# Kernel tuning notes

Measured on AMD Instinct MI355X. Metric: run time of the kernel, lower is better.

The kernel has to match this reference:

```python
import jax, jax.numpy as jnp
import numpy as np

N_NODES = 50000
N_EDGES = 400000
D_IN = 128
D_H = 128
N_CLASSES = 20
N_GRAPHS = 256
EPS_BN = 1e-5


def _lin_params(key, d_in, d_out, scale=0.05):
    kw, kb = jax.random.split(key)
    W = jax.random.normal(kw, (d_in, d_out), jnp.float32) * scale
    b = jax.random.normal(kb, (d_out,), jnp.float32) * scale
    return W, b


def setup_inputs() -> dict:
    key = jax.random.key(0)
    ks = jax.random.split(key, 20)
    inp = {
        "x": jax.random.normal(ks[0], (N_NODES, D_IN), jnp.float32),
        "edge_index": jax.random.randint(ks[1], (2, N_EDGES), 0, N_NODES, jnp.int32),
        "batch": jnp.sort(jax.random.randint(ks[2], (N_NODES,), 0, N_GRAPHS, jnp.int32)),
    }
    kidx = 3
    for li, d_in in zip((1, 2, 3), (D_IN, D_H, D_H)):
        for nm in ("q", "k", "v", "s"):
            W, b = _lin_params(ks[kidx], d_in, D_H)
            kidx += 1
            inp[f"W{nm}{li}"] = W
            inp[f"b{nm}{li}"] = b
        inp[f"gamma{li}"] = jnp.ones((D_H,), jnp.float32)
        inp[f"beta{li}"] = jnp.zeros((D_H,), jnp.float32)
    Wl, bl = _lin_params(ks[kidx], D_H, N_CLASSES)
    inp["Wlin"] = Wl
    inp["blin"] = bl
    return inp


def _segment_softmax(logits, seg, n):
    m = jax.ops.segment_max(logits, seg, num_segments=n)
    e = jnp.exp(logits - m[seg])
    s = jax.ops.segment_sum(e, seg, num_segments=n)
    return e / (s[seg] + 1e-16)


def _transformer_conv(x, src, dst, Wq, bq, Wk, bk, Wv, bv, Ws, bs):
    # heads=1, concat=True, root_weight=True (PyG TransformerConv defaults)
    q = x @ Wq + bq  # [N, d]
    k = x @ Wk + bk
    v = x @ Wv + bv
    d = q.shape[-1]
    logits = jnp.sum(q[dst] * k[src], axis=-1) / jnp.sqrt(jnp.float32(d))  # [E]
    alpha = _segment_softmax(logits, dst, x.shape[0])
    out = jax.ops.segment_sum(alpha[:, None] * v[src], dst, num_segments=x.shape[0])
    return out + x @ Ws + bs


def _batch_norm(x, gamma, beta):
    mu = jnp.mean(x, axis=0)
    var = jnp.var(x, axis=0)
    return gamma * (x - mu) * jax.lax.rsqrt(var + EPS_BN) + beta


def _global_mean_pool(x, batch, n_graphs):
    sums = jax.ops.segment_sum(x, batch, num_segments=n_graphs)
    cnt = jax.ops.segment_sum(jnp.ones((x.shape[0],), x.dtype), batch, num_segments=n_graphs)
    return sums / jnp.maximum(cnt, 1.0)[:, None]


def reference(x, edge_index, batch,
              Wq1, bq1, Wk1, bk1, Wv1, bv1, Ws1, bs1, gamma1, beta1,
              Wq2, bq2, Wk2, bk2, Wv2, bv2, Ws2, bs2, gamma2, beta2,
              Wq3, bq3, Wk3, bk3, Wv3, bv3, Ws3, bs3, gamma3, beta3,
              Wlin, blin):
    src, dst = edge_index[0], edge_index[1]
    h = _transformer_conv(x, src, dst, Wq1, bq1, Wk1, bk1, Wv1, bv1, Ws1, bs1)
    h = jax.nn.relu(_batch_norm(h, gamma1, beta1))  # dropout inactive (eval)
    h = _transformer_conv(h, src, dst, Wq2, bq2, Wk2, bk2, Wv2, bv2, Ws2, bs2)
    h = jax.nn.relu(_batch_norm(h, gamma2, beta2))
    h = _transformer_conv(h, src, dst, Wq3, bq3, Wk3, bk3, Wv3, bv3, Ws3, bs3)
    h = jax.nn.relu(_batch_norm(h, gamma3, beta3))
    g = _global_mean_pool(h, batch, N_GRAPHS)  # [G, d]
    return g @ Wlin + blin  # [G, num_classes]
```

## Files before the change

### kernel.cpp

```cpp
#include <hip/hip_runtime.h>

#define N_NODES 50000
#define N_EDGES 400000
#define DH 128
#define N_GRAPHS 256

#define SCAN_CHUNK 512
#define N_CHUNKS ((N_NODES + SCAN_CHUNK - 1) / SCAN_CHUNK)
#define ATTN_BLOCKS ((N_NODES + 15) / 16)
#define POOL_CHUNKS ((N_NODES + 63) / 64)
#define PSLOTS 16

typedef __bf16 bf16x8 __attribute__((ext_vector_type(8)));
typedef float f32x4 __attribute__((ext_vector_type(4)));
typedef _Float16 f16x2 __attribute__((ext_vector_type(2)));
typedef _Float16 f16x8 __attribute__((ext_vector_type(8)));

#define DEV __device__ __forceinline__

#if defined(__has_builtin)
#if __has_builtin(__builtin_amdgcn_fdot2)
#define HAS_FDOT2 1
#endif
#endif

DEV float fdot2acc(f16x2 a, f16x2 b, float c) {
#ifdef HAS_FDOT2
  return __builtin_amdgcn_fdot2(a, b, c, false);
#else
  return (float)a.x * (float)b.x + (float)a.y * (float)b.y + c;
#endif
}

DEV unsigned short f2bf(float f) {
  union { float f; unsigned int i; } v; v.f = f;
  unsigned int x = v.i;
  unsigned int r = (x + 0x7fffu + ((x >> 16) & 1u)) >> 16;
  return (unsigned short)r;
}

struct WPtrs { const float* w[12]; };

__global__ void repack_kernel(WPtrs wp, unsigned short* __restrict__ WB) {
  int mat = blockIdx.y;
  int m = blockIdx.x * 256 + threadIdx.x;
  int j = m & 7;
  int lane = (m >> 3) & 63;
  int ct = (m >> 9) & 7;
  int kk = m >> 12;
  int i = kk * 32 + (lane >> 4) * 8 + j;
  int o = ct * 16 + (lane & 15);
  WB[mat * 16384 + m] = f2bf(wp.w[mat][i * 128 + o]);
}

__global__ void deg_count(const int* __restrict__ ei, int* __restrict__ deg, int E) {
  int e = blockIdx.x * 256 + threadIdx.x;
  if (e < E) atomicAdd(&deg[ei[E + e]], 1);
}

__global__ __launch_bounds__(256) void scan_sum(const int* __restrict__ deg,
                                                int* __restrict__ partials, int N) {
  __shared__ int red[256];
  int b = blockIdx.x, t = threadIdx.x;
  int base = b * SCAN_CHUNK + t * 2;
  int s = 0;
  if (base + 1 < N) { int2 v = *reinterpret_cast<const int2*>(deg + base); s = v.x + v.y; }
  else if (base < N) s = deg[base];
  red[t] = s;
  __syncthreads();
  for (int off = 128; off; off >>= 1) {
    if (t < off) red[t] += red[t + off];
    __syncthreads();
  }
  if (t == 0) partials[b] = red[0];
}

__global__ __launch_bounds__(256) void scan_apply(const int* __restrict__ deg,
                                                  const int* __restrict__ partials,
                                                  int* __restrict__ rowptr,
                                                  int* __restrict__ cursor, int N, int E) {
  __shared__ int s[256];
  __shared__ int prefSh;
  int b = blockIdx.x, t = threadIdx.x;

  s[t] = (t < b) ? partials[t] : 0;
  __syncthreads();
  for (int off = 128; off; off >>= 1) {
    if (t < off) s[t] += s[t + off];
    __syncthreads();
  }
  if (t == 0) prefSh = s[0];
  __syncthreads();
  int pref = prefSh;
  __syncthreads();

  int base = b * SCAN_CHUNK + t * 2;
  int d0 = 0, d1 = 0;
  if (base + 1 < N) { int2 v = *reinterpret_cast<const int2*>(deg + base); d0 = v.x; d1 = v.y; }
  else if (base < N) d0 = deg[base];
  int local = d0 + d1;
  s[t] = local;
  __syncthreads();
  for (int off = 1; off < 256; off <<= 1) {
    int o = (t >= off) ? s[t - off] : 0;
    __syncthreads();
    s[t] += o;
    __syncthreads();
  }
  int offp = pref + s[t] - local;
  if (base < N)     { rowptr[base] = offp;          cursor[base] = offp; }
  if (base + 1 < N) { rowptr[base + 1] = offp + d0; cursor[base + 1] = offp + d0; }
  if (b == 0 && t == 0) rowptr[N] = E;
}

__global__ void csr_scatter(const int* __restrict__ ei, int* __restrict__ cursor,
                            int* __restrict__ adj, int E) {
  int e = blockIdx.x * 256 + threadIdx.x;
  if (e < E) {
    int dst = ei[E + e];
    int pos = atomicAdd(&cursor[dst], 1);
    adj[pos] = ei[e];
  }
}

__global__ __launch_bounds__(256) void adj_sort16(const int* __restrict__ rowptr,
                                                  int* __restrict__ adj, int N) {
  __shared__ int buf[16 * 32];
  int t = threadIdx.x;
  int g = t >> 4, l = t & 15;
  int n = blockIdx.x * 16 + g;
  bool valid = n < N;
  int p0 = 0, d = 0;
  if (valid) { p0 = rowptr[n]; d = rowptr[n + 1] - p0; }
  if (__builtin_expect(d > 32, 0)) {
    if (l == 0) {
      for (int i = p0 + 1; i < p0 + d; ++i) {
        int v = adj[i]; int j = i - 1;
        while (j >= p0 && adj[j] > v) { adj[j + 1] = adj[j]; --j; }
        adj[j + 1] = v;
      }
    }
    d = 0;
  }
  int a0 = (l < d) ? adj[p0 + l] : 0x7fffffff;
  int a1 = (16 + l < d) ? adj[p0 + 16 + l] : 0x7fffffff;
  int r0 = 0, r1 = 0;
#pragma unroll
  for (int i = 0; i < 16; ++i) {
    int v0 = __shfl(a0, i, 16);
    int v1 = __shfl(a1, i, 16);
    r0 += (v0 < a0) || (v0 == a0 && i < l);
    r0 += (v1 < a0);
    r1 += (v0 <= a1);
    r1 += (v1 < a1) || (v1 == a1 && i < l);
  }
  if (l < d)      buf[g * 32 + r0] = a0;
  if (16 + l < d) buf[g * 32 + r1] = a1;
  __syncthreads();
  if (l < d)      adj[p0 + l]      = buf[g * 32 + l];
  if (16 + l < d) adj[p0 + 16 + l] = buf[g * 32 + 16 + l];
}

struct GemmOut { _Float16* Y[4]; const float* bias[4]; int ldY[4]; };

#define LDP 136

__global__ __launch_bounds__(256) void gemm_proj(
    const float* __restrict__ Xf,
    const _Float16* __restrict__ Hin,
    const float* __restrict__ scale, const float* __restrict__ shift,
    const unsigned short* __restrict__ WB4,
    GemmOut go, int useBN, int N)
{
  __shared__ __align__(16) unsigned short xs[64 * LDP];

  const int t = threadIdx.x;
  const int rowBase = blockIdx.x * 64;
  const int igc = (t & 15) * 8;

  if (useBN) {
    float4 sc0 = *reinterpret_cast<const float4*>(scale + igc);
    float4 sc1 = *reinterpret_cast<const float4*>(scale + igc + 4);
    float4 sh0 = *reinterpret_cast<const float4*>(shift + igc);
    float4 sh1 = *reinterpret_cast<const float4*>(shift + igc + 4);
#pragma unroll
    for (int j = 0; j < 4; ++j) {
      int v = t + 256 * j;
      int r = v >> 4;
      int grow = rowBase + r;
      ushort4 o0 = make_ushort4(0, 0, 0, 0), o1 = make_ushort4(0, 0, 0, 0);
      if (grow < N) {
        f16x8 hv = *reinterpret_cast<const f16x8*>(Hin + (size_t)grow * 128 + igc);
        o0.x = f2bf(fmaxf((float)hv[0] * sc0.x + sh0.x, 0.f));
        o0.y = f2bf(fmaxf((float)hv[1] * sc0.y + sh0.y, 0.f));
        o0.z = f2bf(fmaxf((float)hv[2] * sc0.z + sh0.z, 0.f));
        o0.w = f2bf(fmaxf((float)hv[3] * sc0.w + sh0.w, 0.f));
        o1.x = f2bf(fmaxf((float)hv[4] * sc1.x + sh1.x, 0.f));
        o1.y = f2bf(fmaxf((float)hv[5] * sc1.y + sh1.y, 0.f));
        o1.z = f2bf(fmaxf((float)hv[6] * sc1.z + sh1.z, 0.f));
        o1.w = f2bf(fmaxf((float)hv[7] * sc1.w + sh1.w, 0.f));
      }
      *reinterpret_cast<ushort4*>(&xs[r * LDP + igc]) = o0;
      *reinterpret_cast<ushort4*>(&xs[r * LDP + igc + 4]) = o1;
    }
  } else {
#pragma unroll
    for (int j = 0; j < 4; ++j) {
      int v = t + 256 * j;
      int r = v >> 4;
      int grow = rowBase + r;
      ushort4 o0 = make_ushort4(0, 0, 0, 0), o1 = make_ushort4(0, 0, 0, 0);
      if (grow < N) {
        float4 a = *reinterpret_cast<const float4*>(Xf + (size_t)grow * 128 + igc);
        float4 b = *reinterpret_cast<const float4*>(Xf + (size_t)grow * 128 + igc + 4);
        o0.x = f2bf(a.x); o0.y = f2bf(a.y); o0.z = f2bf(a.z); o0.w = f2bf(a.w);
        o1.x = f2bf(b.x); o1.y = f2bf(b.y); o1.z = f2bf(b.z); o1.w = f2bf(b.w);
      }
      *reinterpret_cast<ushort4*>(&xs[r * LDP + igc]) = o0;
      *reinterpret_cast<ushort4*>(&xs[r * LDP + igc + 4]) = o1;
    }
  }
  __syncthreads();

  const int wave = t >> 6;
  const int lane = t & 63;
  const int ln16 = lane & 15;
  const int quad = lane >> 4;
  const int r0 = wave * 16;

  bf16x8 afrag[4];
#pragma unroll
  for (int kk = 0; kk < 4; ++kk)
    afrag[kk] = *reinterpret_cast<const bf16x8*>(&xs[(r0 + ln16) * LDP + kk * 32 + quad * 8]);
  __syncthreads();

  for (int proj = 0; proj < 4; ++proj) {
    const unsigned short* __restrict__ WB = WB4 + proj * 16384;
    const float* __restrict__ bias = go.bias[proj];

    f32x4 acc[8] = {};
#pragma unroll
    for (int kk = 0; kk < 4; ++kk) {
#pragma unroll
      for (int ct = 0; ct < 8; ++ct) {
        bf16x8 b = *reinterpret_cast<const bf16x8*>(WB + ((kk * 8 + ct) * 64 + lane) * 8);
        acc[ct] = __builtin_amdgcn_mfma_f32_16x16x32_bf16(afrag[kk], b, acc[ct], 0, 0, 0);
      }
    }

    _Float16* __restrict__ Yh = go.Y[proj];
    const int ldY = go.ldY[proj];
#pragma unroll
    for (int ct = 0; ct < 8; ++ct) {
      int col = ct * 16 + ln16;
      float bv = bias[col];
#pragma unroll
      for (int reg = 0; reg < 4; ++reg) {
        _Float16 hv = (_Float16)(acc[ct][reg] + bv);
        xs[(r0 + quad * 4 + reg) * LDP + col] = __builtin_bit_cast(unsigned short, hv);
      }
    }
#pragma unroll
    for (int pass = 0; pass < 4; ++pass) {
      int rl = (lane >> 4) + pass * 4;
      int grow = rowBase + r0 + rl;
      f16x8 v = *reinterpret_cast<const f16x8*>(&xs[(r0 + rl) * LDP + ln16 * 8]);
      if (grow < N)
        *reinterpret_cast<f16x8*>(&Yh[(size_t)grow * ldY + ln16 * 8]) = v;
    }
  }
}

__global__ __launch_bounds__(256) void node_attn(
    const int* __restrict__ rowptr, const int* __restrict__ adj,
    const _Float16* __restrict__ Q, const _Float16* __restrict__ KV,
    _Float16* __restrict__ H, float* __restrict__ Pbuf, int N)
{
  __shared__ float lsum[16][132];
  __shared__ float lsq[16][132];
  int t = threadIdx.x;
  int w = t >> 4, lane = t & 15;
  int n = blockIdx.x * 16 + w;
  bool valid = n < N;
  int nn = valid ? n : 0;
  int p0 = 0, p1 = 0;
  if (valid) { p0 = rowptr[n]; p1 = rowptr[n + 1]; }
  int d = p1 - p0;

  f16x8 qv = *reinterpret_cast<const f16x8*>(Q + (size_t)nn * 128 + lane * 8);
  f16x8 hh = *reinterpret_cast<const f16x8*>(H + (size_t)nn * 128 + lane * 8);
  f16x2 q0 = {qv[0], qv[1]}, q1 = {qv[2], qv[3]}, q2 = {qv[4], qv[5]}, q3 = {qv[6], qv[7]};

  const float rsqd = 0.08838834764831845f;
  float m = -INFINITY, s = 0.f;
  float acc[8] = {};

#define EDGE1(SRC) do {                                                        \
    const _Float16* bp_ = KV + (size_t)(SRC) * 256 + lane * 8;                 \
    f16x8 ke_ = *reinterpret_cast<const f16x8*>(bp_);                          \
    f16x8 ve_ = *reinterpret_cast<const f16x8*>(bp_ + 128);                    \
    float dd_ = fdot2acc(q0, (f16x2){ke_[0], ke_[1]},                          \
                fdot2acc(q1, (f16x2){ke_[2], ke_[3]},                          \
                fdot2acc(q2, (f16x2){ke_[4], ke_[5]},                          \
                fdot2acc(q3, (f16x2){ke_[6], ke_[7]}, 0.f))));                 \
    for (int off_ = 8; off_; off_ >>= 1) dd_ += __shfl_xor(dd_, off_, 16);     \
    float ll_ = dd_ * rsqd;                                                    \
    float mn_ = fmaxf(m, ll_);                                                 \
    float sc_ = __expf(m - mn_);                                               \
    float w0_ = __expf(ll_ - mn_);                                             \
    for (int i_ = 0; i_ < 8; ++i_) acc[i_] = acc[i_] * sc_ + w0_ * (float)ve_[i_]; \
    s = s * sc_ + w0_;                                                         \
    m = mn_;                                                                   \
  } while (0)

  if (__builtin_expect(d <= 32, 1)) {
    int aLo = (lane < d) ? adj[p0 + lane] : 0;
    int aHi = (16 + lane < d) ? adj[p0 + 16 + lane] : 0;
    int e = 0;
    for (; e + 1 < d; e += 2) {
      int s0 = __shfl((e     < 16) ? aLo : aHi, (e    ) & 15, 16);
      int s1 = __shfl((e + 1 < 16) ? aLo : aHi, (e + 1) & 15, 16);
      const _Float16* b0 = KV + (size_t)s0 * 256 + lane * 8;
      const _Float16* b1 = KV + (size_t)s1 * 256 + lane * 8;
      f16x8 k0 = *reinterpret_cast<const f16x8*>(b0);
      f16x8 k1 = *reinterpret_cast<const f16x8*>(b1);
      f16x8 v0 = *reinterpret_cast<const f16x8*>(b0 + 128);
      f16x8 v1 = *reinterpret_cast<const f16x8*>(b1 + 128);
      float d0 = fdot2acc(q0, (f16x2){k0[0], k0[1]},
                 fdot2acc(q1, (f16x2){k0[2], k0[3]},
                 fdot2acc(q2, (f16x2){k0[4], k0[5]},
                 fdot2acc(q3, (f16x2){k0[6], k0[7]}, 0.f))));
      float d1 = fdot2acc(q0, (f16x2){k1[0], k1[1]},
                 fdot2acc(q1, (f16x2){k1[2], k1[3]},
                 fdot2acc(q2, (f16x2){k1[4], k1[5]},
                 fdot2acc(q3, (f16x2){k1[6], k1[7]}, 0.f))));
#pragma unroll
      for (int off = 8; off; off >>= 1) {
        d0 += __shfl_xor(d0, off, 16);
        d1 += __shfl_xor(d1, off, 16);
      }
      float l0 = d0 * rsqd;
      float l1 = d1 * rsqd;
      float mn = fmaxf(m, fmaxf(l0, l1));
      float sc = __expf(m - mn);
      float w0 = __expf(l0 - mn);
      float w1 = __expf(l1 - mn);
#pragma unroll
      for (int i = 0; i < 8; ++i)
        acc[i] = acc[i] * sc + w0 * (float)v0[i] + w1 * (float)v1[i];
      s = s * sc + w0 + w1;
      m = mn;
    }
    if (e < d) {
      int sE = __shfl((e < 16) ? aLo : aHi, e & 15, 16);
      EDGE1(sE);
    }
  } else {
    for (int p = p0; p < p1; ++p) { int sE = adj[p]; EDGE1(sE); }
  }
#undef EDGE1

  float h[8];
#pragma unroll
  for (int i = 0; i < 8; ++i) h[i] = 0.f;
  if (valid) {
    float inv = 1.0f / (s + 1e-16f);
    f16x8 ho;
#pragma unroll
    for (int i = 0; i < 8; ++i) {
      h[i] = (float)hh[i] + acc[i] * inv;
      ho[i] = (_Float16)h[i];
    }
    *reinterpret_cast<f16x8*>(H + (size_t)n * 128 + lane * 8) = ho;
  }

#pragma unroll
  for (int i = 0; i < 8; i += 4) {
    float4 hv = make_float4(h[i], h[i + 1], h[i + 2], h[i + 3]);
    float4 h2 = make_float4(hv.x * hv.x, hv.y * hv.y, hv.z * hv.z, hv.w * hv.w);
    *reinterpret_cast<float4*>(&lsum[w][lane * 8 + i]) = hv;
    *reinterpret_cast<float4*>(&lsq[w][lane * 8 + i]) = h2;
  }
  __syncthreads();

  int f = t & 127;
  float a = 0.f;
  if (t < 128) {
#pragma unroll
    for (int n16 = 0; n16 < 16; ++n16) a += lsum[n16][f];
  } else {
#pragma unroll
    for (int n16 = 0; n16 < 16; ++n16) a += lsq[n16][f];
  }
  Pbuf[(size_t)blockIdx.x * 256 + t] = a;
}

__global__ __launch_bounds__(256) void bn_fused(
    const float* __restrict__ Pbuf, float* __restrict__ bnpart,
    const float* __restrict__ gamma, const float* __restrict__ beta,
    float* __restrict__ scale, float* __restrict__ shift,
    int* __restrict__ ticket, int N)
{
  __shared__ float red[256];
  __shared__ int amLast;
  int t = threadIdx.x;
  {
    float s0 = 0.f, s1 = 0.f, s2 = 0.f, s3 = 0.f;
    int r = blockIdx.x;
    for (; r + 192 < ATTN_BLOCKS; r += 256) {
      s0 += Pbuf[(size_t)(r      ) * 256 + t];
      s1 += Pbuf[(size_t)(r +  64) * 256 + t];
      s2 += Pbuf[(size_t)(r + 128) * 256 + t];
      s3 += Pbuf[(size_t)(r + 192) * 256 + t];
    }
    for (; r < ATTN_BLOCKS; r += 64) s0 += Pbuf[(size_t)r * 256 + t];
    bnpart[blockIdx.x * 256 + t] = s0 + s1 + s2 + s3;
  }
  __threadfence();
  if (t == 0) amLast = (atomicAdd(ticket, 1) == 63);
  __syncthreads();
  if (!amLast) return;
  __threadfence();

  float s0 = 0.f, s1 = 0.f, s2 = 0.f, s3 = 0.f;
#pragma unroll
  for (int r = 0; r < 64; r += 4) {
    s0 += bnpart[(r + 0) * 256 + t];
    s1 += bnpart[(r + 1) * 256 + t];
    s2 += bnpart[(r + 2) * 256 + t];
    s3 += bnpart[(r + 3) * 256 + t];
  }
  red[t] = s0 + s1 + s2 + s3;
  __syncthreads();
  if (t < 128) {
    float mean = red[t] / (float)N;
    float var = red[t + 128] / (float)N - mean * mean;
    var = fmaxf(var, 0.f);
    float sc = gamma[t] * rsqrtf(var + 1e-5f);
    scale[t] = sc;
    shift[t] = beta[t] - mean * sc;
  }
}

__global__ __launch_bounds__(256) void pool_partial(
    const _Float16* __restrict__ H, const float* __restrict__ scale,
    const float* __restrict__ shift, const int* __restrict__ batch,
    float* __restrict__ partial, int N)
{
  int f = threadIdx.x & 127, parity = threadIdx.x >> 7;
  int base = blockIdx.x * 64;
  int lim = min(base + 64, N);
  float sc = scale[f], sh = shift[f];
  int slot = ((blockIdx.x & 7) << 1) | parity;
  int curg = -1; float s = 0.f;
  for (int row = base + parity; row < lim; row += 2) {
    int g = batch[row];
    if (g != curg) {
      if (curg >= 0) partial[(size_t)((curg << 4) | slot) * 128 + f] = s;
      curg = g; s = 0.f;
    }
    s += fmaxf((float)H[(size_t)row * 128 + f] * sc + sh, 0.f);
  }
  if (curg >= 0) partial[(size_t)((curg << 4) | slot) * 128 + f] = s;
}

__global__ __launch_bounds__(128) void final_linear(
    const float* __restrict__ partial, const int* __restrict__ batch,
    const float* __restrict__ Wlin, const float* __restrict__ blin,
    float* __restrict__ out, int N)
{
  __shared__ float pf[128];
  int g = blockIdx.x;
  int t = threadIdx.x;
  float s = 0.f;
#pragma unroll
  for (int sl = 0; sl < PSLOTS; ++sl)
    s += partial[(size_t)((g << 4) | sl) * 128 + t];
  pf[t] = s;
  __syncthreads();
  int lo = 0, hi = N;
  while (lo < hi) { int mid = (lo + hi) >> 1; if (batch[mid] < g) lo = mid + 1; else hi = mid; }
  int start = lo;
  hi = N;
  while (lo < hi) { int mid = (lo + hi) >> 1; if (batch[mid] < g + 1) lo = mid + 1; else hi = mid; }
  float inv = 1.0f / fmaxf((float)(lo - start), 1.f);
  if (t < 20) {
    float acc = 0.f;
#pragma unroll 4
    for (int i = 0; i < 128; ++i)
      acc += pf[i] * Wlin[i * 20 + t];
    out[g * 20 + t] = acc * inv + blin[t];
  }
}

extern "C" void kernel_launch(void* const* d_in, const int* in_sizes, int n_in,
                              void* d_out, int out_size, void* d_ws, size_t ws_size,
                              hipStream_t stream)
{
  const int N = N_NODES, E = N_EDGES, G = N_GRAPHS;

  const float* x = (const float*)d_in[0];
  const int* ei = (const int*)d_in[1];
  const int* batch = (const int*)d_in[2];
  const float* Wlin = (const float*)d_in[33];
  const float* blin = (const float*)d_in[34];

  char* ws = (char*)d_ws;
  size_t off = 0;
  auto alloc = [&](size_t bytes) -> void* {
    void* p = ws + off;
    off = (off + bytes + 255) & ~(size_t)255;
    return p;
  };
  unsigned short* WB = (unsigned short*)alloc(12 * 16384 * sizeof(unsigned short));
  _Float16* Qh  = (_Float16*)alloc((size_t)N * 128 * 2);
  _Float16* KVh = (_Float16*)alloc((size_t)N * 256 * 2);
  _Float16* Hh  = (_Float16*)alloc((size_t)N * 128 * 2);
  int* rowptr   = (int*)alloc((size_t)(N + 1) * 4);
  int* cursor   = (int*)alloc((size_t)N * 4);
  int* adj      = (int*)alloc((size_t)E * 4);
  int* partials = (int*)alloc((size_t)N_CHUNKS * 4);
  float* Pbuf   = (float*)alloc((size_t)ATTN_BLOCKS * 256 * 4);
  float* bnpart = (float*)alloc((size_t)64 * 256 * 4);
  float* scale  = (float*)alloc(128 * 4);
  float* shift  = (float*)alloc(128 * 4);
  size_t zoff = off;
  int* deg      = (int*)alloc((size_t)N * 4);
  int* tickets  = (int*)alloc(256);
  float* ppool  = (float*)alloc((size_t)G * PSLOTS * 128 * 4);
  size_t zbytes = off - zoff;

  WPtrs wp;
  for (int L = 0; L < 3; ++L) {
    wp.w[L * 4 + 0] = (const float*)d_in[3 + L * 10 + 0];
    wp.w[L * 4 + 1] = (const float*)d_in[3 + L * 10 + 2];
    wp.w[L * 4 + 2] = (const float*)d_in[3 + L * 10 + 4];
    wp.w[L * 4 + 3] = (const float*)d_in[3 + L * 10 + 6];
  }
  repack_kernel<<<dim3(64, 12), 256, 0, stream>>>(wp, WB);

  hipMemsetAsync(deg, 0, zbytes, stream);
  deg_count<<<(E + 255) / 256, 256, 0, stream>>>(ei, deg, E);
  scan_sum<<<N_CHUNKS, 256, 0, stream>>>(deg, partials, N);
  scan_apply<<<N_CHUNKS, 256, 0, stream>>>(deg, partials, rowptr, cursor, N, E);
  csr_scatter<<<(E + 255) / 256, 256, 0, stream>>>(ei, cursor, adj, E);
  adj_sort16<<<ATTN_BLOCKS, 256, 0, stream>>>(rowptr, adj, N);

  for (int L = 0; L < 3; ++L) {
    GemmOut go;
    go.Y[0] = Qh;        go.ldY[0] = 128;
    go.Y[1] = KVh;       go.ldY[1] = 256;
    go.Y[2] = KVh + 128; go.ldY[2] = 256;
    go.Y[3] = Hh;        go.ldY[3] = 128;
    go.bias[0] = (const float*)d_in[3 + L * 10 + 1];
    go.bias[1] = (const float*)d_in[3 + L * 10 + 3];
    go.bias[2] = (const float*)d_in[3 + L * 10 + 5];
    go.bias[3] = (const float*)d_in[3 + L * 10 + 7];
    gemm_proj<<<(N + 63) / 64, 256, 0, stream>>>(
        x, Hh, scale, shift, WB + L * 4 * 16384, go, (L > 0) ? 1 : 0, N);

    node_attn<<<ATTN_BLOCKS, 256, 0, stream>>>(rowptr, adj, Qh, KVh, Hh, Pbuf, N);

    bn_fused<<<64, 256, 0, stream>>>(Pbuf, bnpart,
        (const float*)d_in[3 + L * 10 + 8],
        (const float*)d_in[3 + L * 10 + 9],
        scale, shift, tickets + L, N);

    if (L == 2) {
      pool_partial<<<POOL_CHUNKS, 256, 0, stream>>>(Hh, scale, shift, batch, ppool, N);
      final_linear<<<G, 128, 0, stream>>>(ppool, batch, Wlin, blin, (float*)d_out, N);
    }
  }
}
```

Before: 433.0 us.

## Fold BN reduction, adj sort and zeroing into neighbouring kernels to cut launches

Removes the separate bn_fused kernel by having the last-arriving 64 blocks of the next GEMM (or pool) kernel compute the batch-norm statistics, while every other block spin-waits on a release flag. It also runs the adjacency sort as extra blocks of the first GEMM launch and replaces the memset plus weight-repack kernel with one combined kernel. The aim is to remove several kernel launches and their gaps. The cost is an in-kernel spin barrier. It relies on the late-ranked blocks being resident while the others spin, which risks stalls or deadlock if they are not.

New measurement: 913.2 us. 2.11x slower.

```diff
diff --git a/kernel.cpp b/kernel.cpp
--- a/kernel.cpp
+++ b/kernel.cpp
@@ -9,6 +9,7 @@
 #define N_CHUNKS ((N_NODES + SCAN_CHUNK - 1) / SCAN_CHUNK)
 #define ATTN_BLOCKS ((N_NODES + 15) / 16)
 #define POOL_CHUNKS ((N_NODES + 63) / 64)
+#define NB_GEMM ((N_NODES + 63) / 64)
 #define PSLOTS 16
 
 typedef __bf16 bf16x8 __attribute__((ext_vector_type(8)));
@@ -41,16 +42,27 @@
 
 struct WPtrs { const float* w[12]; };
 
-__global__ void repack_kernel(WPtrs wp, unsigned short* __restrict__ WB) {
-  int mat = blockIdx.y;
-  int m = blockIdx.x * 256 + threadIdx.x;
-  int j = m & 7;
-  int lane = (m >> 3) & 63;
-  int ct = (m >> 9) & 7;
-  int kk = m >> 12;
-  int i = kk * 32 + (lane >> 4) * 8 + j;
-  int o = ct * 16 + (lane & 15);
-  WB[mat * 16384 + m] = f2bf(wp.w[mat][i * 128 + o]);
+__global__ __launch_bounds__(256) void repack_zero(
+    WPtrs wp, unsigned short* __restrict__ WB,
+    int* __restrict__ deg, int* __restrict__ ctrl, float* __restrict__ ppool,
+    int N)
+{
+  const int T = 768 * 256;
+  int gtid = blockIdx.x * 256 + threadIdx.x;
+  for (int m = gtid; m < 12 * 16384; m += T) {
+    int mat = m >> 14;
+    int mm = m & 16383;
+    int j = mm & 7;
+    int lane = (mm >> 3) & 63;
+    int ct = (mm >> 9) & 7;
+    int kk = mm >> 12;
+    int i = kk * 32 + (lane >> 4) * 8 + j;
+    int o = ct * 16 + (lane & 15);
+    WB[m] = f2bf(wp.w[mat][i * 128 + o]);
+  }
+  for (int i = gtid; i < N; i += T) deg[i] = 0;
+  if (gtid < 64) ctrl[gtid] = 0;
+  for (int i = gtid; i < N_GRAPHS * PSLOTS * 128; i += T) ppool[i] = 0.f;
 }
 
 __global__ void deg_count(const int* __restrict__ ei, int* __restrict__ deg, int E) {
@@ -123,12 +135,12 @@
   }
 }
 
-__global__ __launch_bounds__(256) void adj_sort16(const int* __restrict__ rowptr,
-                                                  int* __restrict__ adj, int N) {
-  __shared__ int buf[16 * 32];
+DEV void adj_sort_body(const int* __restrict__ rowptr, int* __restrict__ adj,
+                       int nodeBase, int N) {
+  __shared__ int sbuf[16 * 32];
   int t = threadIdx.x;
   int g = t >> 4, l = t & 15;
-  int n = blockIdx.x * 16 + g;
+  int n = nodeBase + g;
   bool valid = n < N;
   int p0 = 0, d = 0;
   if (valid) { p0 = rowptr[n]; d = rowptr[n + 1] - p0; }
@@ -154,25 +166,95 @@
     r1 += (v0 <= a1);
     r1 += (v1 < a1) || (v1 == a1 && i < l);
   }
-  if (l < d)      buf[g * 32 + r0] = a0;
-  if (16 + l < d) buf[g * 32 + r1] = a1;
-  __syncthreads();
-  if (l < d)      adj[p0 + l]      = buf[g * 32 + l];
-  if (16 + l < d) adj[p0 + 16 + l] = buf[g * 32 + 16 + l];
+  if (l < d)      sbuf[g * 32 + r0] = a0;
+  if (16 + l < d) sbuf[g * 32 + r1] = a1;
+  __syncthreads();
+  if (l < d)      adj[p0 + l]      = sbuf[g * 32 + l];
+  if (16 + l < d) adj[p0 + 16 + l] = sbuf[g * 32 + 16 + l];
+}
+
+DEV void bn_prologue(const float* __restrict__ Pbuf, float* __restrict__ bnpart,
+                     const float* __restrict__ gamma, const float* __restrict__ beta,
+                     float* __restrict__ scale, float* __restrict__ shift,
+                     int* __restrict__ sync, int nb, int N) {
+  __shared__ int rankSh;
+  __shared__ int lastSh;
+  __shared__ float red[256];
+  int t = threadIdx.x;
+  if (t == 0) rankSh = atomicAdd(&sync[0], 1);
+  __syncthreads();
+  int rank = rankSh;
+  if (rank >= nb - 64 && rank < nb) {
+    int slot = rank - (nb - 64);
+    float s0 = 0.f, s1 = 0.f, s2 = 0.f, s3 = 0.f;
+    int r = slot;
+    for (; r + 192 < ATTN_BLOCKS; r += 256) {
+      s0 += Pbuf[(size_t)(r      ) * 256 + t];
+      s1 += Pbuf[(size_t)(r +  64) * 256 + t];
+      s2 += Pbuf[(size_t)(r + 128) * 256 + t];
+      s3 += Pbuf[(size_t)(r + 192) * 256 + t];
+    }
+    for (; r < ATTN_BLOCKS; r += 64) s0 += Pbuf[(size_t)r * 256 + t];
+    bnpart[slot * 256 + t] = s0 + s1 + s2 + s3;
+    __threadfence();
+    if (t == 0) lastSh = (atomicAdd(&sync[1], 1) == 63);
+    __syncthreads();
+    if (lastSh) {
+      __threadfence();
+      float v0 = 0.f, v1 = 0.f, v2 = 0.f, v3 = 0.f;
+#pragma unroll
+      for (int q = 0; q < 64; q += 4) {
+        v0 += bnpart[(q + 0) * 256 + t];
+        v1 += bnpart[(q + 1) * 256 + t];
+        v2 += bnpart[(q + 2) * 256 + t];
+        v3 += bnpart[(q + 3) * 256 + t];
+      }
+      red[t] = v0 + v1 + v2 + v3;
+      __syncthreads();
+      if (t < 128) {
+        float mean = red[t] / (float)N;
+        float var = red[t + 128] / (float)N - mean * mean;
+        var = fmaxf(var, 0.f);
+        float sc = gamma[t] * rsqrtf(var + 1e-5f);
+        scale[t] = sc;
+        shift[t] = beta[t] - mean * sc;
+      }
+      __syncthreads();
+      __threadfence();
+      if (t == 0)
+        __hip_atomic_store(&sync[2], 1, __ATOMIC_RELEASE, __HIP_MEMORY_SCOPE_AGENT);
+    }
+  }
+  if (t == 0) {
+    while (__hip_atomic_load(&sync[2], __ATOMIC_ACQUIRE,
+                             __HIP_MEMORY_SCOPE_AGENT) == 0) {}
+  }
+  __syncthreads();
 }
 
 struct GemmOut { _Float16* Y[4]; const float* bias[4]; int ldY[4]; };
 
 #define LDP 136
 
-__global__ __launch_bounds__(256) void gemm_proj(
+__global__ __launch_bounds__(256, 4) void gemm_proj(
     const float* __restrict__ Xf,
     const _Float16* __restrict__ Hin,
-    const float* __restrict__ scale, const float* __restrict__ shift,
+    const float* __restrict__ Pbuf, float* __restrict__ bnpart,
+    const float* __restrict__ gamma, const float* __restrict__ beta,
+    float* __restrict__ scale, float* __restrict__ shift,
+    int* __restrict__ sync,
     const unsigned short* __restrict__ WB4,
-    GemmOut go, int useBN, int N)
+    GemmOut go, int useBN, int N, int nbGemm,
+    const int* __restrict__ rowptr, int* __restrict__ adj)
 {
   __shared__ __align__(16) unsigned short xs[64 * LDP];
+
+  if ((int)blockIdx.x >= nbGemm) {
+    adj_sort_body(rowptr, adj, ((int)blockIdx.x - nbGemm) * 16, N);
+    return;
+  }
+  if (useBN)
+    bn_prologue(Pbuf, bnpart, gamma, beta, scale, shift, sync, nbGemm, N);
 
   const int t = threadIdx.x;
   const int rowBase = blockIdx.x * 64;
@@ -395,58 +477,16 @@
   Pbuf[(size_t)blockIdx.x * 256 + t] = a;
 }
 
-__global__ __launch_bounds__(256) void bn_fused(
+__global__ __launch_bounds__(256) void pool_partial(
+    const _Float16* __restrict__ H,
     const float* __restrict__ Pbuf, float* __restrict__ bnpart,
     const float* __restrict__ gamma, const float* __restrict__ beta,
     float* __restrict__ scale, float* __restrict__ shift,
-    int* __restrict__ ticket, int N)
+    int* __restrict__ sync,
+    const int* __restrict__ batch, float* __restrict__ partial, int N)
 {
-  __shared__ float red[256];
-  __shared__ int amLast;
-  int t = threadIdx.x;
-  {
-    float s0 = 0.f, s1 = 0.f, s2 = 0.f, s3 = 0.f;
-    int r = blockIdx.x;
-    for (; r + 192 < ATTN_BLOCKS; r += 256) {
-      s0 += Pbuf[(size_t)(r      ) * 256 + t];
-      s1 += Pbuf[(size_t)(r +  64) * 256 + t];
-      s2 += Pbuf[(size_t)(r + 128) * 256 + t];
-      s3 += Pbuf[(size_t)(r + 192) * 256 + t];
-    }
-    for (; r < ATTN_BLOCKS; r += 64) s0 += Pbuf[(size_t)r * 256 + t];
-    bnpart[blockIdx.x * 256 + t] = s0 + s1 + s2 + s3;
-  }
-  __threadfence();
-  if (t == 0) amLast = (atomicAdd(ticket, 1) == 63);
-  __syncthreads();
-  if (!amLast) return;
-  __threadfence();
-
-  float s0 = 0.f, s1 = 0.f, s2 = 0.f, s3 = 0.f;
-#pragma unroll
-  for (int r = 0; r < 64; r += 4) {
-    s0 += bnpart[(r + 0) * 256 + t];
-    s1 += bnpart[(r + 1) * 256 + t];
-    s2 += bnpart[(r + 2) * 256 + t];
-    s3 += bnpart[(r + 3) * 256 + t];
-  }
-  red[t] = s0 + s1 + s2 + s3;
-  __syncthreads();
-  if (t < 128) {
-    float mean = red[t] / (float)N;
-    float var = red[t + 128] / (float)N - mean * mean;
-    var = fmaxf(var, 0.f);
-    float sc = gamma[t] * rsqrtf(var + 1e-5f);
-    scale[t] = sc;
-    shift[t] = beta[t] - mean * sc;
-  }
-}
-
-__global__ __launch_bounds__(256) void pool_partial(
-    const _Float16* __restrict__ H, const float* __restrict__ scale,
-    const float* __restrict__ shift, const int* __restrict__ batch,
-    float* __restrict__ partial, int N)
-{
+  bn_prologue(Pbuf, bnpart, gamma, beta, scale, shift, sync, POOL_CHUNKS, N);
+
   int f = threadIdx.x & 127, parity = threadIdx.x >> 7;
   int base = blockIdx.x * 64;
   int lim = min(base + 64, N);
@@ -524,11 +564,11 @@
   float* bnpart = (float*)alloc((size_t)64 * 256 * 4);
   float* scale  = (float*)alloc(128 * 4);
   float* shift  = (float*)alloc(128 * 4);
-  size_t zoff = off;
   int* deg      = (int*)alloc((size_t)N * 4);
-  int* tickets  = (int*)alloc(256);
+  int* ctrl     = (int*)alloc(64 * 4);
   float* ppool  = (float*)alloc((size_t)G * PSLOTS * 128 * 4);
-  size_t zbytes = off - zoff;
+
+  int* snc[3] = { ctrl + 16, ctrl + 20, ctrl + 24 };
 
   WPtrs wp;
   for (int L = 0; L < 3; ++L) {
@@ -537,14 +577,12 @@
     wp.w[L * 4 + 2] = (const float*)d_in[3 + L * 10 + 4];
     wp.w[L * 4 + 3] = (const float*)d_in[3 + L * 10 + 6];
   }
-  repack_kernel<<<dim3(64, 12), 256, 0, stream>>>(wp, WB);
-
-  hipMemsetAsync(deg, 0, zbytes, stream);
+
+  repack_zero<<<768, 256, 0, stream>>>(wp, WB, deg, ctrl, ppool, N);
   deg_count<<<(E + 255) / 256, 256, 0, stream>>>(ei, deg, E);
   scan_sum<<<N_CHUNKS, 256, 0, stream>>>(deg, partials, N);
   scan_apply<<<N_CHUNKS, 256, 0, stream>>>(deg, partials, rowptr, cursor, N, E);
   csr_scatter<<<(E + 255) / 256, 256, 0, stream>>>(ei, cursor, adj, E);
-  adj_sort16<<<ATTN_BLOCKS, 256, 0, stream>>>(rowptr, adj, N);
 
   for (int L = 0; L < 3; ++L) {
     GemmOut go;
@@ -556,19 +594,27 @@
     go.bias[1] = (const float*)d_in[3 + L * 10 + 3];
     go.bias[2] = (const float*)d_in[3 + L * 10 + 5];
     go.bias[3] = (const float*)d_in[3 + L * 10 + 7];
-    gemm_proj<<<(N + 63) / 64, 256, 0, stream>>>(
-        x, Hh, scale, shift, WB + L * 4 * 16384, go, (L > 0) ? 1 : 0, N);
+
+    if (L == 0) {
+      gemm_proj<<<NB_GEMM + ATTN_BLOCKS, 256, 0, stream>>>(
+          x, Hh, nullptr, nullptr, nullptr, nullptr, scale, shift, snc[0],
+          WB, go, 0, N, NB_GEMM, rowptr, adj);
+    } else {
+      gemm_proj<<<NB_GEMM, 256, 0, stream>>>(
+          x, Hh, Pbuf, bnpart,
+          (const float*)d_in[3 + (L - 1) * 10 + 8],
+          (const float*)d_in[3 + (L - 1) * 10 + 9],
+          scale, shift, snc[L - 1],
+          WB + L * 4 * 16384, go, 1, N, NB_GEMM, nullptr, nullptr);
+    }
 
     node_attn<<<ATTN_BLOCKS, 256, 0, stream>>>(rowptr, adj, Qh, KVh, Hh, Pbuf, N);
-
-    bn_fused<<<64, 256, 0, stream>>>(Pbuf, bnpart,
-        (const float*)d_in[3 + L * 10 + 8],
-        (const float*)d_in[3 + L * 10 + 9],
-        scale, shift, tickets + L, N);
-
-    if (L == 2) {
-      pool_partial<<<POOL_CHUNKS, 256, 0, stream>>>(Hh, scale, shift, batch, ppool, N);
-      final_linear<<<G, 128, 0, stream>>>(ppool, batch, Wlin, blin, (float*)d_out, N);
-    }
-  }
-}
+  }
+
+  pool_partial<<<POOL_CHUNKS, 256, 0, stream>>>(
+      Hh, Pbuf, bnpart,
+      (const float*)d_in[3 + 2 * 10 + 8],
+      (const float*)d_in[3 + 2 * 10 + 9],
+      scale, shift, snc[2], batch, ppool, N);
+  final_linear<<<G, 128, 0, stream>>>(ppool, batch, Wlin, blin, (float*)d_out, N);
+}
```
